# Performance work log

Measured on AMD Instinct MI355X. Metric: run time of the kernel, lower is better.

The kernel has to match this reference:

```python
import jax, jax.numpy as jnp
import numpy as np


def setup_inputs() -> dict:
    key = jax.random.key(0)
    k1, k2 = jax.random.split(key)
    B, C, H, W = 4, 256, 64, 64
    hw = 1024  # hs = ws = 32, rate = H/hs = 2
    ori_x = jax.random.normal(k1, (B, C, H, W), dtype=jnp.float32)
    scores = jax.random.uniform(k2, (B, hw, hw), dtype=jnp.float32)
    alpha = jnp.ones((1,), dtype=jnp.float32)
    return {"ori_x": ori_x, "scores": scores, "alpha": alpha}


def reference(ori_x, scores, alpha):
    # GroupConvAttention forward for H=W=64 (no bilinear resize branch taken,
    # matching the torch code's else-branch), rate even (no extra rep-pad).
    B, C, H, W = ori_x.shape
    hw = scores.shape[2]
    hs = int(np.sqrt(hw)); ws = hs
    rate = H // hs               # 2
    vk = 2 * rate                # vksize = 4
    pad = rate // 2              # vpadding = 1 (rate even)

    # extract_patches: ReplicationPad2d(pad) + unfold(kernel=vk, stride=rate)
    x_pad = jnp.pad(ori_x, ((0, 0), (0, 0), (pad, pad), (pad, pad)), mode="edge")
    # gather index grids: patch (m,n), intra-patch (u,v)
    ri = (jnp.arange(hs) * rate)[:, None] + jnp.arange(vk)[None, :]  # [hs, vk]
    ci = (jnp.arange(ws) * rate)[:, None] + jnp.arange(vk)[None, :]  # [ws, vk]
    R = ri[:, None, :, None]   # [hs,1,vk,1]
    Cc = ci[None, :, None, :]  # [1,ws,1,vk]
    value = x_pad[:, :, R, Cc]  # [B, C, hs, ws, vk, vk]

    # conv_transpose2d(scores_, value, stride=rate, padding=pad, groups=B)
    # == per query grid cell (Q,R): combined patch = sum_p scores[b,q,p]*value[b,p]
    s = scores.reshape(B, hs, ws, hs, ws)  # [b, Qy, Qx, my, mx]
    P = jnp.einsum("bQRmn,bcmnuv->bcQRuv", s, value)  # [B,C,hs,ws,vk,vk]

    # overlap-add patches at stride `rate` into padded canvas, then crop padding
    canvas = jnp.zeros((B, C, (hs - 1) * rate + vk, (ws - 1) * rate + vk), P.dtype)
    canvas = canvas.at[:, :, R, Cc].add(P)
    y = canvas[:, :, pad:pad + H, pad:pad + W] / 4.0

    return ori_x + y * alpha
```

## Files before the change

### kernel.cpp

```cpp
#include <hip/hip_runtime.h>
#include <hip/hip_bf16.h>
#include <hip/hip_fp16.h>

#define BB 4
#define CC 256
#define HH 64
#define WW 64
#define QRN 1024
#define KN  1024
#define KDIM 1152
#define TROWS 1089

typedef _Float16 f16x8 __attribute__((ext_vector_type(8)));
typedef float f32x4 __attribute__((ext_vector_type(4)));
typedef float f32x16 __attribute__((ext_vector_type(16)));

#define TP_ELEMS ((size_t)BB * TROWS * KDIM)
#define BP_ELEMS ((size_t)16 * CC * KDIM)


__device__ __forceinline__
void process_qr(const float* __restrict__ sb, _Float16* __restrict__ T,
                int b, int qr, int t) {
    const int Qa = (qr * 993) >> 15;
    const int Ra = qr - 33 * Qa;
    const bool q0 = (Qa < 32), q1 = (Qa >= 1);
    const bool r0 = (Ra < 32), r1 = (Ra >= 1);
    const float* rb00 = sb + ((size_t)((Qa)     * 32 + (Ra)))     * KN;
    const float* rb01 = sb + ((size_t)((Qa)     * 32 + (Ra - 1))) * KN;
    const float* rb10 = sb + ((size_t)((Qa - 1) * 32 + (Ra)))     * KN;
    const float* rb11 = sb + ((size_t)((Qa - 1) * 32 + (Ra - 1))) * KN;
    _Float16* trow = T + ((size_t)b * TROWS + qr) * KDIM;

    float v[5];
    #pragma unroll
    for (int j = 0; j < 5; ++j) {
        const int k = j * 256 + t;
        v[j] = 0.f;
        if (k < KDIM) {
            const int mp = (k * 993) >> 15;
            const int np = k - 33 * mp;
            const bool m0 = (mp < 32), m1 = (mp >= 1) && (mp < 33);
            const bool n0 = (np < 32), n1 = (np >= 1);
            const int col = (mp << 5) + np;
            if (q0 & r0 & m0 & n0) v[j] += rb00[col];
            if (q0 & r1 & m0 & n1) v[j] += rb01[col - 1];
            if (q1 & r0 & m1 & n0) v[j] += rb10[col - 32];
            if (q1 & r1 & m1 & n1) v[j] += rb11[col - 33];
        }
    }
    #pragma unroll
    for (int j = 0; j < 5; ++j) {
        const int k = j * 256 + t;
        if (k < KDIM) trow[k] = (_Float16)v[j];
    }
}

#define T_BLOCKS 545
#define PER_B    705
#define TB_NWG   (BB * PER_B)

__global__ __launch_bounds__(256)
void build_TB(const float* __restrict__ s, const float* __restrict__ x,
              _Float16* __restrict__ T, _Float16* __restrict__ Bp) {
    const int orig = blockIdx.x;
    const int xcd = orig & 7, pos = orig >> 3;
    const int q = TB_NWG / 8, r = TB_NWG % 8;
    const int wgid =
        (xcd < r ? xcd * (q + 1) : r * (q + 1) + (xcd - r) * q) + pos;

    const int b = wgid / PER_B;
    const int rem = wgid - b * PER_B;
    const int t = threadIdx.x;

    if (rem < T_BLOCKS) {
        const float* sb = s + (size_t)b * QRN * KN;
        const int qr0 = rem * 2;
        process_qr(sb, T, b, qr0, t);
        if (qr0 + 1 < TROWS) process_qr(sb, T, b, qr0 + 1, t);
    } else {
        const int u = rem - T_BLOCKS;
        const int rest = u / 5;
        const int kc = u - rest * 5;
        const int cls = rest >> 3, cg = rest & 7;
        const int k = kc * 256 + t;
        if (k >= KDIM) return;
        const int ph = cls >> 1, pw = cls & 1;
        const int ua = 1 - ph, va = 1 - pw;
        const int bc = b * 4 + cls;

        const int mp = (k * 993) >> 15;
        const int np = k - 33 * mp;
        int rr = 2 * mp + ua - 1; rr = min(max(rr, 0), HH - 1);
        int cc2 = 2 * np + va - 1; cc2 = min(max(cc2, 0), WW - 1);
        const int off = rr * WW + cc2;

        const float* xb = x + ((size_t)b * CC + cg * 32) * HH * WW;
        _Float16* bpb = Bp + ((size_t)bc * CC + cg * 32) * KDIM + k;

        #pragma unroll 8
        for (int i = 0; i < 32; ++i) {
            bpb[(size_t)i * KDIM] = (_Float16)xb[(size_t)i * HH * WW + off];
        }
    }
}

#define A_SLOT 520
#define B_SLOT 1040
#define A_BUF  (8 * A_SLOT)
#define B_BUF  (8 * B_SLOT)
#define NSTEP  18
__global__ __launch_bounds__(256)
void gemm_f16(const _Float16* __restrict__ T,
              const _Float16* __restrict__ Bp,
              const float* __restrict__ orix,
              const float* __restrict__ alphap,
              float* __restrict__ out) {
    __shared__ __align__(16) char smem[49920];
    _Float16* AmB = (_Float16*)smem;
    _Float16* BnB = AmB + 2 * A_BUF;
    float*    ex  = (float*)smem;

    const int lin = blockIdx.x + 4 * (blockIdx.y + 8 * blockIdx.z);
    const int wid = (lin & 7) * 64 + (lin >> 3);
    const int bc  = wid >> 5;
    const int byy = (wid >> 2) & 7;
    const int bxx = wid & 3;

    const int b = bc >> 2, cls = bc & 3;
    const int ph = cls >> 1, pw = cls & 1;
    const int c0  = bxx * 64;
    const int px0 = byy * 128;

    const int t = threadIdx.x;
    const int wv = t >> 6, l = t & 63;
    const int lr = l & 31;
    const int lh = l >> 5;
    const int wc = wv & 1;
    const int ks = wv >> 1;

    const _Float16* Ag = Bp + ((size_t)bc * CC + c0) * KDIM;
    const _Float16* Tg = T + (size_t)b * TROWS * KDIM;

    const int st_r    = t >> 3;
    const int st_slot = t & 7;
    const int kb0     = st_slot * 8;
    int trowv[4];
    #pragma unroll
    for (int r2 = 0; r2 < 4; ++r2) {
        const int px = px0 + r2 * 32 + st_r;
        trowv[r2] = ((px >> 5) + ph) * 33 + (px & 31) + pw;
    }

    f32x16 acc[2][2];
    #pragma unroll
    for (int i = 0; i < 2; ++i)
        #pragma unroll
        for (int j = 0; j < 2; ++j)
            acc[i][j] = (f32x16)(0.f);

    f16x8 rga[2][2], rgb[2][4];

    #pragma unroll
    for (int s2 = 0; s2 < 2; ++s2) {
        const size_t kb = (size_t)s2 * 64 + kb0;
        rga[s2][0] = *reinterpret_cast<const f16x8*>(Ag + (size_t)st_r * KDIM + kb);
        rga[s2][1] = *reinterpret_cast<const f16x8*>(Ag + (size_t)(st_r + 32) * KDIM + kb);
        #pragma unroll
        for (int r2 = 0; r2 < 4; ++r2)
            rgb[s2][r2] = *reinterpret_cast<const f16x8*>(
                Tg + (size_t)trowv[r2] * KDIM + kb);
    }
    *reinterpret_cast<f16x8*>(&AmB[st_slot * A_SLOT + st_r * 8]) = rga[0][0];
    *reinterpret_cast<f16x8*>(&AmB[st_slot * A_SLOT + (st_r + 32) * 8]) = rga[0][1];
    #pragma unroll
    for (int r2 = 0; r2 < 4; ++r2)
        *reinterpret_cast<f16x8*>(
            &BnB[st_slot * B_SLOT + (r2 * 32 + st_r) * 8]) = rgb[0][r2];
    asm volatile("s_waitcnt lgkmcnt(0)" ::: "memory");
    __builtin_amdgcn_s_barrier();

    #pragma unroll
    for (int ts = 0; ts < NSTEP; ++ts) {
        const int cur = ts & 1;
        if (ts + 2 < NSTEP) {
            const int sl = ts & 1;
            const size_t kb = (size_t)(ts + 2) * 64 + kb0;
            rga[sl][0] = *reinterpret_cast<const f16x8*>(Ag + (size_t)st_r * KDIM + kb);
            rga[sl][1] = *reinterpret_cast<const f16x8*>(Ag + (size_t)(st_r + 32) * KDIM + kb);
            #pragma unroll
            for (int r2 = 0; r2 < 4; ++r2)
                rgb[sl][r2] = *reinterpret_cast<const f16x8*>(
                    Tg + (size_t)trowv[r2] * KDIM + kb);
        }

        f16x8 af[2][2], bf[2][2];
        #pragma unroll
        for (int kk = 0; kk < 2; ++kk) {
            const int slot = ks * 4 + kk * 2 + lh;
            #pragma unroll
            for (int mt = 0; mt < 2; ++mt)
                af[mt][kk] = *reinterpret_cast<const f16x8*>(
                    &AmB[cur * A_BUF + slot * A_SLOT + (mt * 32 + lr) * 8]);
            #pragma unroll
            for (int nt2 = 0; nt2 < 2; ++nt2)
                bf[nt2][kk] = *reinterpret_cast<const f16x8*>(
                    &BnB[cur * B_BUF + slot * B_SLOT +
                         (wc * 64 + nt2 * 32 + lr) * 8]);
        }
        __builtin_amdgcn_s_setprio(1);
        #pragma unroll
        for (int kk = 0; kk < 2; ++kk)
            #pragma unroll
            for (int mt = 0; mt < 2; ++mt)
                #pragma unroll
                for (int nt2 = 0; nt2 < 2; ++nt2)
                    acc[mt][nt2] = __builtin_amdgcn_mfma_f32_32x32x16_f16(
                        af[mt][kk], bf[nt2][kk], acc[mt][nt2], 0, 0, 0);
        __builtin_amdgcn_s_setprio(0);

        if (ts + 1 < NSTEP) {
            const int ns = (ts + 1) & 1, nb = cur ^ 1;
            *reinterpret_cast<f16x8*>(
                &AmB[nb * A_BUF + st_slot * A_SLOT + st_r * 8]) = rga[ns][0];
            *reinterpret_cast<f16x8*>(
                &AmB[nb * A_BUF + st_slot * A_SLOT + (st_r + 32) * 8]) = rga[ns][1];
            #pragma unroll
            for (int r2 = 0; r2 < 4; ++r2)
                *reinterpret_cast<f16x8*>(
                    &BnB[nb * B_BUF + st_slot * B_SLOT +
                         (r2 * 32 + st_r) * 8]) = rgb[ns][r2];
        }
        asm volatile("s_waitcnt lgkmcnt(0)" ::: "memory");
        __builtin_amdgcn_s_barrier();
    }

    if (ks == 1) {
        #pragma unroll
        for (int mt = 0; mt < 2; ++mt)
            #pragma unroll
            for (int nt2 = 0; nt2 < 2; ++nt2)
                #pragma unroll
                for (int r2 = 0; r2 < 16; ++r2)
                    ex[((((mt * 2 + nt2) * 2 + wc) * 16) + r2) * 64 + l] =
                        acc[mt][nt2][r2];
    }
    asm volatile("s_waitcnt lgkmcnt(0)" ::: "memory");
    __builtin_amdgcn_s_barrier();

    if (ks == 0) {
        const float scale = 0.25f * alphap[0];
        #pragma unroll
        for (int mt = 0; mt < 2; ++mt) {
            #pragma unroll
            for (int nt2 = 0; nt2 < 2; ++nt2) {
                #pragma unroll
                for (int r2 = 0; r2 < 16; ++r2) {
                    float vsum = acc[mt][nt2][r2] +
                        ex[((((mt * 2 + nt2) * 2 + wc) * 16) + r2) * 64 + l];
                    int c  = c0 + mt * 32 + (r2 & 3) + 8 * (r2 >> 2) + 4 * lh;
                    int px = px0 + wc * 64 + nt2 * 32 + lr;
                    int hh = px >> 5, ww2 = px & 31;
                    int h = 2 * hh + ph, wp = 2 * ww2 + pw;
                    size_t idx = (((size_t)b * CC + c) * HH + h) * WW + wp;
                    out[idx] = orix[idx] + scale * vsum;
                }
            }
        }
    }
}

#define TILE_M 64
#define TILE_N 64
#define TILE_K 16

__global__ void copy_kernel(const float* __restrict__ src,
                            float* __restrict__ dst, int n4) {
    int i = blockIdx.x * blockDim.x + threadIdx.x;
    if (i < n4)
        reinterpret_cast<float4*>(dst)[i] =
            reinterpret_cast<const float4*>(src)[i];
}

__global__ void transpose_kernel(const float* __restrict__ x,
                                 float* __restrict__ xT) {
    __shared__ float tile[32][33];
    int bh = blockIdx.z;
    int b = bh >> 6, h = bh & 63;
    int c0 = blockIdx.y * 32, w0 = blockIdx.x * 32;
    int tw = threadIdx.x & 31;
    int tc = threadIdx.x >> 5;
    #pragma unroll
    for (int i = 0; i < 4; ++i) {
        int c = tc + i * 8;
        tile[c][tw] = x[(((size_t)b * CC + c0 + c) * HH + h) * WW + w0 + tw];
    }
    __syncthreads();
    int tcw = threadIdx.x & 31;
    int twr = threadIdx.x >> 5;
    #pragma unroll
    for (int i = 0; i < 4; ++i) {
        int w = twr + i * 8;
        xT[(((size_t)b * HH + h) * WW + w0 + w) * CC + c0 + tcw] = tile[tcw][w];
    }
}

__global__ __launch_bounds__(256)
void pgemm_scatter(const float* __restrict__ scores,
                   const float* __restrict__ xT,
                   const float* __restrict__ x,
                   const float* __restrict__ alpha,
                   float* __restrict__ out,
                   int use_xt) {
    __shared__ float As[TILE_K][TILE_M];
    __shared__ float Bs[TILE_K][TILE_N];

    const int b      = blockIdx.z;
    const int tile_n = blockIdx.x;
    const int m0     = blockIdx.y * TILE_M;
    const int uv     = tile_n >> 2;
    const int u      = uv >> 2, v = uv & 3;
    const int c0     = (tile_n & 3) * 64;

    const int t  = threadIdx.x;
    const int tx = t & 15;
    const int ty = t >> 4;

    float acc[4][4] = {};
    const float* sb = scores + (size_t)b * QRN * KN;

    for (int k0 = 0; k0 < KN; k0 += TILE_K) {
        {
            int mr = t >> 2;
            int kc = (t & 3) * 4;
            float4 av = *reinterpret_cast<const float4*>(
                sb + (size_t)(m0 + mr) * KN + k0 + kc);
            As[kc + 0][mr] = av.x;
            As[kc + 1][mr] = av.y;
            As[kc + 2][mr] = av.z;
            As[kc + 3][mr] = av.w;
        }
        {
            int kr = t >> 4;
            int kg = k0 + kr;
            int m  = kg >> 5, n = kg & 31;
            int rr = 2 * m + u - 1; rr = min(max(rr, 0), HH - 1);
            int cc = 2 * n + v - 1; cc = min(max(cc, 0), WW - 1);
            int ccol = (t & 15) * 4;
            if (use_xt) {
                float4 bv = *reinterpret_cast<const float4*>(
                    xT + ((((size_t)b * HH + rr) * WW + cc) * CC) + c0 + ccol);
                Bs[kr][ccol + 0] = bv.x;
                Bs[kr][ccol + 1] = bv.y;
                Bs[kr][ccol + 2] = bv.z;
                Bs[kr][ccol + 3] = bv.w;
            } else {
                #pragma unroll
                for (int j = 0; j < 4; ++j) {
                    int c = c0 + ccol + j;
                    Bs[kr][ccol + j] =
                        x[(((size_t)b * CC + c) * HH + rr) * WW + cc];
                }
            }
        }
        __syncthreads();

        #pragma unroll
        for (int k = 0; k < TILE_K; ++k) {
            float a4[4], b4[4];
            *reinterpret_cast<float4*>(a4) =
                *reinterpret_cast<const float4*>(&As[k][ty * 4]);
            *reinterpret_cast<float4*>(b4) =
                *reinterpret_cast<const float4*>(&Bs[k][tx * 4]);
            #pragma unroll
            for (int i = 0; i < 4; ++i)
                #pragma unroll
                for (int j = 0; j < 4; ++j)
                    acc[i][j] += a4[i] * b4[j];
        }
        __syncthreads();
    }

    const float scale = alpha[0] * 0.25f;
    #pragma unroll
    for (int i = 0; i < 4; ++i) {
        int qr = m0 + ty * 4 + i;
        int Q = qr >> 5, R = qr & 31;
        int h = 2 * Q + u - 1;
        int w = 2 * R + v - 1;
        if (h < 0 || h >= HH || w < 0 || w >= WW) continue;
        #pragma unroll
        for (int j = 0; j < 4; ++j) {
            int c = c0 + tx * 4 + j;
            atomicAdd(&out[(((size_t)b * CC + c) * HH + h) * WW + w],
                      acc[i][j] * scale);
        }
    }
}

extern "C" void kernel_launch(void* const* d_in, const int* in_sizes, int n_in,
                              void* d_out, int out_size, void* d_ws,
                              size_t ws_size, hipStream_t stream) {
    const float* ori_x  = (const float*)d_in[0];
    const float* scores = (const float*)d_in[1];
    const float* alpha  = (const float*)d_in[2];
    float* out = (float*)d_out;

    const size_t need_fast = (TP_ELEMS + BP_ELEMS) * sizeof(_Float16);

    if (ws_size >= need_fast) {
        _Float16* T  = (_Float16*)d_ws;
        _Float16* Bp = T + TP_ELEMS;

        build_TB<<<dim3(TB_NWG), 256, 0, stream>>>(scores, ori_x, T, Bp);
        gemm_f16<<<dim3(4, 8, 16), 256, 0, stream>>>(T, Bp, ori_x, alpha, out);
    } else {
        float* xT = (float*)d_ws;
        const size_t xt_bytes = (size_t)BB * HH * WW * CC * sizeof(float);
        const int use_xt = (ws_size >= xt_bytes) ? 1 : 0;

        copy_kernel<<<(BB * CC * HH * WW / 4 + 255) / 256, 256, 0, stream>>>(
            ori_x, out, BB * CC * HH * WW / 4);
        if (use_xt)
            transpose_kernel<<<dim3(WW / 32, CC / 32, BB * HH), 256, 0,
                               stream>>>(ori_x, xT);
        pgemm_scatter<<<dim3(16, 16, BB), 256, 0, stream>>>(
            scores, xT, ori_x, alpha, out, use_xt);
    }
}
```

Before: 49.00 us.

## Use direct global-to-LDS loads with a 4-stage ring buffer in GEMM

The GEMM main loop stops staging tiles through registers and instead issues global_load_lds (direct-to-LDS) transfers into a four-deep ring buffer with three stages in flight. The K step is halved to 32 (36 iterations), and a single vmcnt wait plus barrier per step replaces the register-to-LDS store path. This aims to cut VGPR pressure and LDS write instructions and to hide more global latency. The cost is more barriers per K, a smaller MFMA batch per step, and an unpadded LDS layout that may cause bank conflicts.

```diff
diff --git a/kernel.cpp b/kernel.cpp
--- a/kernel.cpp
+++ b/kernel.cpp
@@ -12,7 +12,6 @@
 #define TROWS 1089
 
 typedef _Float16 f16x8 __attribute__((ext_vector_type(8)));
-typedef float f32x4 __attribute__((ext_vector_type(4)));
 typedef float f32x16 __attribute__((ext_vector_type(16)));
 
 #define TP_ELEMS ((size_t)BB * TROWS * KDIM)
@@ -105,21 +104,24 @@
     }
 }
 
-#define A_SLOT 520
-#define B_SLOT 1040
-#define A_BUF  (8 * A_SLOT)
-#define B_BUF  (8 * B_SLOT)
-#define NSTEP  18
+__device__ __forceinline__ void gload16(const _Float16* g, _Float16* l) {
+    __builtin_amdgcn_global_load_lds(
+        (const __attribute__((address_space(1))) unsigned int*)g,
+        (__attribute__((address_space(3))) unsigned int*)l, 16, 0, 0);
+}
+
+#define NSTEP  36
+#define ABUF_H 2048
+#define BBUF_H 4096
+#define B_BASE 8192
 __global__ __launch_bounds__(256)
 void gemm_f16(const _Float16* __restrict__ T,
               const _Float16* __restrict__ Bp,
               const float* __restrict__ orix,
               const float* __restrict__ alphap,
               float* __restrict__ out) {
-    __shared__ __align__(16) char smem[49920];
-    _Float16* AmB = (_Float16*)smem;
-    _Float16* BnB = AmB + 2 * A_BUF;
-    float*    ex  = (float*)smem;
+    __shared__ __align__(16) _Float16 smem_h[24576];
+    float* ex = (float*)smem_h;
 
     const int lin = blockIdx.x + 4 * (blockIdx.y + 8 * blockIdx.z);
     const int wid = (lin & 7) * 64 + (lin >> 3);
@@ -133,24 +135,32 @@
     const int px0 = byy * 128;
 
     const int t = threadIdx.x;
-    const int wv = t >> 6, l = t & 63;
+    const int w = t >> 6, l = t & 63;
     const int lr = l & 31;
     const int lh = l >> 5;
-    const int wc = wv & 1;
-    const int ks = wv >> 1;
+    const int wc = w & 1;
+    const int ks = w >> 1;
 
     const _Float16* Ag = Bp + ((size_t)bc * CC + c0) * KDIM;
     const _Float16* Tg = T + (size_t)b * TROWS * KDIM;
 
-    const int st_r    = t >> 3;
-    const int st_slot = t & 7;
-    const int kb0     = st_slot * 8;
-    int trowv[4];
-    #pragma unroll
-    for (int r2 = 0; r2 < 4; ++r2) {
-        const int px = px0 + r2 * 32 + st_r;
-        trowv[r2] = ((px >> 5) + ph) * 33 + (px & 31) + pw;
-    }
+    const int rowB = (w & 1) * 64 + l;
+    const int pxB = px0 + rowB;
+    const int trowB = ((pxB >> 5) + ph) * 33 + (pxB & 31) + pw;
+
+    const _Float16* srcA = Ag + (size_t)l * KDIM + w * 8;
+    const _Float16* srcB = Tg + (size_t)trowB * KDIM + (w >> 1) * 8;
+    _Float16* dstA = smem_h + w * 512 + l * 8;
+    _Float16* dstB = smem_h + B_BASE + w * 512 + l * 8;
+
+    #define ISSUE(ts2)                                                     \
+        do {                                                               \
+            const int _bf = (ts2) & 3;                                     \
+            const int _k0 = (ts2) * 32;                                    \
+            gload16(srcA + _k0, dstA + _bf * ABUF_H);                      \
+            gload16(srcB + _k0, dstB + _bf * BBUF_H);                      \
+            gload16(srcB + _k0 + 16, dstB + _bf * BBUF_H + 2048);          \
+        } while (0)
 
     f32x16 acc[2][2];
     #pragma unroll
@@ -159,81 +169,33 @@
         for (int j = 0; j < 2; ++j)
             acc[i][j] = (f32x16)(0.f);
 
-    f16x8 rga[2][2], rgb[2][4];
-
-    #pragma unroll
-    for (int s2 = 0; s2 < 2; ++s2) {
-        const size_t kb = (size_t)s2 * 64 + kb0;
-        rga[s2][0] = *reinterpret_cast<const f16x8*>(Ag + (size_t)st_r * KDIM + kb);
-        rga[s2][1] = *reinterpret_cast<const f16x8*>(Ag + (size_t)(st_r + 32) * KDIM + kb);
-        #pragma unroll
-        for (int r2 = 0; r2 < 4; ++r2)
-            rgb[s2][r2] = *reinterpret_cast<const f16x8*>(
-                Tg + (size_t)trowv[r2] * KDIM + kb);
-    }
-    *reinterpret_cast<f16x8*>(&AmB[st_slot * A_SLOT + st_r * 8]) = rga[0][0];
-    *reinterpret_cast<f16x8*>(&AmB[st_slot * A_SLOT + (st_r + 32) * 8]) = rga[0][1];
-    #pragma unroll
-    for (int r2 = 0; r2 < 4; ++r2)
-        *reinterpret_cast<f16x8*>(
-            &BnB[st_slot * B_SLOT + (r2 * 32 + st_r) * 8]) = rgb[0][r2];
-    asm volatile("s_waitcnt lgkmcnt(0)" ::: "memory");
+    ISSUE(0); ISSUE(1); ISSUE(2);
+
+    for (int ts = 0; ts < NSTEP; ++ts) {
+        asm volatile("s_waitcnt vmcnt(6)" ::: "memory");
+        __builtin_amdgcn_s_barrier();
+        const int nxt = (ts + 3 < NSTEP) ? ts + 3 : NSTEP - 1;
+        ISSUE(nxt);
+
+        const int bufb = ts & 3;
+        const _Float16* ab = smem_h + bufb * ABUF_H;
+        const _Float16* bb = smem_h + B_BASE + bufb * BBUF_H;
+        const int slot = ks * 2 + lh;
+        f16x8 af0 = *(const f16x8*)(ab + slot * 512 + lr * 8);
+        f16x8 af1 = *(const f16x8*)(ab + slot * 512 + (32 + lr) * 8);
+        f16x8 bf0 = *(const f16x8*)(bb + slot * 1024 + (wc * 64 + lr) * 8);
+        f16x8 bf1 = *(const f16x8*)(bb + slot * 1024 + (wc * 64 + 32 + lr) * 8);
+        __builtin_amdgcn_s_setprio(1);
+        acc[0][0] = __builtin_amdgcn_mfma_f32_32x32x16_f16(af0, bf0, acc[0][0], 0, 0, 0);
+        acc[0][1] = __builtin_amdgcn_mfma_f32_32x32x16_f16(af0, bf1, acc[0][1], 0, 0, 0);
+        acc[1][0] = __builtin_amdgcn_mfma_f32_32x32x16_f16(af1, bf0, acc[1][0], 0, 0, 0);
+        acc[1][1] = __builtin_amdgcn_mfma_f32_32x32x16_f16(af1, bf1, acc[1][1], 0, 0, 0);
+        __builtin_amdgcn_s_setprio(0);
+    }
+    #undef ISSUE
+
+    asm volatile("s_waitcnt vmcnt(0) lgkmcnt(0)" ::: "memory");
     __builtin_amdgcn_s_barrier();
-
-    #pragma unroll
-    for (int ts = 0; ts < NSTEP; ++ts) {
-        const int cur = ts & 1;
-        if (ts + 2 < NSTEP) {
-            const int sl = ts & 1;
-            const size_t kb = (size_t)(ts + 2) * 64 + kb0;
-            rga[sl][0] = *reinterpret_cast<const f16x8*>(Ag + (size_t)st_r * KDIM + kb);
-            rga[sl][1] = *reinterpret_cast<const f16x8*>(Ag + (size_t)(st_r + 32) * KDIM + kb);
-            #pragma unroll
-            for (int r2 = 0; r2 < 4; ++r2)
-                rgb[sl][r2] = *reinterpret_cast<const f16x8*>(
-                    Tg + (size_t)trowv[r2] * KDIM + kb);
-        }
-
-        f16x8 af[2][2], bf[2][2];
-        #pragma unroll
-        for (int kk = 0; kk < 2; ++kk) {
-            const int slot = ks * 4 + kk * 2 + lh;
-            #pragma unroll
-            for (int mt = 0; mt < 2; ++mt)
-                af[mt][kk] = *reinterpret_cast<const f16x8*>(
-                    &AmB[cur * A_BUF + slot * A_SLOT + (mt * 32 + lr) * 8]);
-            #pragma unroll
-            for (int nt2 = 0; nt2 < 2; ++nt2)
-                bf[nt2][kk] = *reinterpret_cast<const f16x8*>(
-                    &BnB[cur * B_BUF + slot * B_SLOT +
-                         (wc * 64 + nt2 * 32 + lr) * 8]);
-        }
-        __builtin_amdgcn_s_setprio(1);
-        #pragma unroll
-        for (int kk = 0; kk < 2; ++kk)
-            #pragma unroll
-            for (int mt = 0; mt < 2; ++mt)
-                #pragma unroll
-                for (int nt2 = 0; nt2 < 2; ++nt2)
-                    acc[mt][nt2] = __builtin_amdgcn_mfma_f32_32x32x16_f16(
-                        af[mt][kk], bf[nt2][kk], acc[mt][nt2], 0, 0, 0);
-        __builtin_amdgcn_s_setprio(0);
-
-        if (ts + 1 < NSTEP) {
-            const int ns = (ts + 1) & 1, nb = cur ^ 1;
-            *reinterpret_cast<f16x8*>(
-                &AmB[nb * A_BUF + st_slot * A_SLOT + st_r * 8]) = rga[ns][0];
-            *reinterpret_cast<f16x8*>(
-                &AmB[nb * A_BUF + st_slot * A_SLOT + (st_r + 32) * 8]) = rga[ns][1];
-            #pragma unroll
-            for (int r2 = 0; r2 < 4; ++r2)
-                *reinterpret_cast<f16x8*>(
-                    &BnB[nb * B_BUF + st_slot * B_SLOT +
-                         (r2 * 32 + st_r) * 8]) = rgb[ns][r2];
-        }
-        asm volatile("s_waitcnt lgkmcnt(0)" ::: "memory");
-        __builtin_amdgcn_s_barrier();
-    }
 
     if (ks == 1) {
         #pragma unroll
```

Measured after the change: 65.19 us. 1.33x slower.
